# Kernel tuning notes

Hardware: AMD Instinct MI355X
Metric: run time of the kernel (lower is better)

## Reference

```python
import jax, jax.numpy as jnp
import numpy as np

RATIO = 4


def setup_inputs() -> dict:
    key = jax.random.key(0)
    ks = jax.random.split(key, 6)
    b, c, hw = 8, 64, 256
    n = (hw // RATIO) ** 2  # 4096
    return {
        "x": jax.random.normal(ks[0], (b, c, hw, hw), dtype=jnp.float32),
        "weight": jax.random.normal(ks[1], (n, n), dtype=jnp.float32) * 0.01,
        "pih_w": jax.random.normal(ks[2], (c, c, 3, 3), dtype=jnp.float32) * 0.05,
        "pih_b": jax.random.normal(ks[3], (c,), dtype=jnp.float32) * 0.05,
        "up_w": jax.random.normal(ks[4], (c, c, 4, 4), dtype=jnp.float32) * 0.05,
        "up_b": jax.random.normal(ks[5], (c,), dtype=jnp.float32) * 0.05,
    }


def reference(x, weight, pih_w, pih_b, up_w, up_b):
    b, c, h, w = x.shape
    identity = x
    # MaxPool2d(ratio)
    xp = jax.lax.reduce_window(x, -jnp.inf, jax.lax.max,
                               (1, 1, RATIO, RATIO), (1, 1, RATIO, RATIO), 'VALID')
    # 3x3 conv, pad 1
    x_pih = jax.lax.conv_general_dilated(
        xp, pih_w, window_strides=(1, 1), padding='SAME',
        dimension_numbers=('NCHW', 'OIHW', 'NCHW')) + pih_b[None, :, None, None]
    x_pih = jax.nn.relu(x_pih).reshape(b, c, -1)  # [b, c, N]
    # F.normalize(p=2, dim=2)
    nrm = jnp.sqrt(jnp.sum(x_pih * x_pih, axis=2, keepdims=True))
    nx = x_pih / jnp.maximum(nrm, 1e-12)
    # channel-channel affinity [b, c, c]
    A = jnp.einsum('bcn,bdn->bcd', nx, nx)
    # vectorized D^{-1/2}, replacing per-batch torch.diag loop
    d = 1.0 / jnp.sqrt(jnp.sum(A, axis=2) + 1e-8)  # [b, c]
    d = jnp.where(jnp.isfinite(d), d, 0.0)
    L = jnp.eye(c, dtype=x.dtype)[None] - d[:, :, None] * A * d[:, None, :]
    # diffusion: L @ x_flat @ W
    xf = xp.reshape(b, c, -1)  # [b, c, N]
    out = jnp.einsum('bcd,bdn->bcn', L, xf)
    out = jnp.einsum('bcn,nm->bcm', out, weight)
    hp, wp = h // RATIO, w // RATIO
    out = out.reshape(b, c, hp, wp)
    # ConvTranspose2d(k=4, s=4): each pixel expands to a 4x4 block
    up = jnp.einsum('bchw,coij->bohiwj', out, up_w).reshape(b, c, h, w)
    up = up + up_b[None, :, None, None]
    return jax.nn.relu(up + identity)
```

## Files before the change

kernel.cpp:

```cpp
#include <hip/hip_runtime.h>

#define NB 8
#define NC 64
#define HW 256
#define HP 64
#define NN 4096

typedef unsigned short u16;
typedef unsigned int u32;
typedef __attribute__((ext_vector_type(8))) short s16x8;
typedef __attribute__((ext_vector_type(8))) unsigned short u16x8;
typedef __attribute__((ext_vector_type(4))) float f32x4;

__device__ __forceinline__ u16 f2bf(float f) {
    unsigned u = __float_as_uint(f);
    return (u16)((u + 0x7fffu + ((u >> 16) & 1u)) >> 16);
}
__device__ __forceinline__ float bf2f(u16 v) {
    return __uint_as_float(((unsigned)v) << 16);
}

#define GLOAD16(gsrc, ldst) \
    __builtin_amdgcn_global_load_lds((const __attribute__((address_space(1))) unsigned int*)(gsrc), \
                                     (__attribute__((address_space(3))) unsigned int*)(ldst), 16, 0, 0)

__global__ __launch_bounds__(256) void prep_k(const float* __restrict__ uw,
                                              const float* __restrict__ pw,
                                              u16* __restrict__ Wb,
                                              u16* __restrict__ Bpack) {
    int bid = blockIdx.x;
    if (bid < 256) {
        int idx = bid * 256 + threadIdx.x;
        int c = idx & 63;
        int n = idx >> 6;
        int o = n >> 4, i = (n >> 2) & 3, j = n & 3;
        Wb[idx] = f2bf(uw[((c * 64 + o) * 4 + i) * 4 + j]);
    } else {
        int idx = (bid - 256) * 256 + threadIdx.x;
        if (idx >= 36864) return;
        int e = idx & 7, l = (idx >> 3) & 63, nf = (idx >> 9) & 3, s = idx >> 11;
        int ch = s & 1, kd = s >> 1;
        int dy = kd / 3, dx = kd % 3;
        int o  = nf * 16 + (l & 15);
        int ci = ch * 32 + (l >> 4) * 8 + e;
        Bpack[idx] = f2bf(pw[((o * 64 + ci) * 3 + dy) * 3 + dx]);
    }
}

__global__ __launch_bounds__(256) void transWb_k(const float* __restrict__ W,
                                                 u16* __restrict__ WTb) {
    __shared__ float tile[64 * 65];
    int k0 = blockIdx.x * 64;
    int n0 = blockIdx.y * 64;
    int t = threadIdx.x;
#pragma unroll
    for (int i = 0; i < 4; ++i) {
        int idx = t + i * 256;
        int r  = idx >> 4;
        int c4 = (idx & 15) * 4;
        float4 v = *(const float4*)&W[(long)(k0 + r) * 4096 + n0 + c4];
        tile[(c4 + 0) * 65 + r] = v.x;
        tile[(c4 + 1) * 65 + r] = v.y;
        tile[(c4 + 2) * 65 + r] = v.z;
        tile[(c4 + 3) * 65 + r] = v.w;
    }
    __syncthreads();
#pragma unroll
    for (int i = 0; i < 2; ++i) {
        int chunk = t + i * 256;
        int nr = chunk >> 3;
        int kc = (chunk & 7) * 8;
        u16x8 o;
#pragma unroll
        for (int j = 0; j < 8; ++j) o[j] = f2bf(tile[nr * 65 + kc + j]);
        *(u16x8*)&WTb[(long)(n0 + nr) * 4096 + k0 + kc] = o;
    }
}

__global__ __launch_bounds__(256) void maxpool_nhwc_k(const float* __restrict__ x,
                                                      u16* __restrict__ xpc) {
    __shared__ u16 tile[64 * 66];
    int bid = blockIdx.x;
    int b = bid >> 6, y = bid & 63;
    int t = threadIdx.x;
    int c = t >> 2, q = t & 3;
    const float* p = x + ((long)(b * 64 + c) * 256 + y * 4) * 256 + q * 64;
#pragma unroll
    for (int i = 0; i < 16; ++i) {
        float m = -3.4e38f;
#pragma unroll
        for (int r = 0; r < 4; ++r) {
            float4 v = *(const float4*)(p + r * 256 + i * 4);
            m = fmaxf(m, fmaxf(fmaxf(v.x, v.y), fmaxf(v.z, v.w)));
        }
        tile[c * 66 + q * 16 + i] = f2bf(m);
    }
    __syncthreads();
    int xo = t >> 2, cp = t & 3;
    u16x8 o0, o1;
#pragma unroll
    for (int e = 0; e < 8; ++e) o0[e] = tile[(cp * 16 + e) * 66 + xo];
#pragma unroll
    for (int e = 0; e < 8; ++e) o1[e] = tile[(cp * 16 + 8 + e) * 66 + xo];
    u16* dst = xpc + ((long)(b * 4096 + y * 64 + xo)) * 64 + cp * 16;
    *(u16x8*)dst = o0;
    *(u16x8*)(dst + 8) = o1;
}

__global__ __launch_bounds__(256) void conv_mfma_k(const u16* __restrict__ xpc,
                                                   const u16* __restrict__ Bpack,
                                                   const float* __restrict__ pb,
                                                   u16* __restrict__ xpihb) {
    __shared__ alignas(16) u16 ldsIn[3 * 66 * 64];
    int bid = blockIdx.x;
    int b = bid >> 6, y = bid & 63;
    int t = threadIdx.x;
    int w = t >> 6, l = t & 63;
    int lr = l & 15, ksub = l >> 4;

    if (t < 48) {
        int r = t >> 4, q = t & 15;
        int off = r * 8448 + (q < 8 ? q * 16 : 8320 + (q - 8) * 16);
        *(u16x8*)((char*)ldsIn + off) = (u16x8){0, 0, 0, 0, 0, 0, 0, 0};
    }
#pragma unroll
    for (int i = 0; i < 6; ++i) {
        int r  = i >> 1;
        int ya = y - 1 + r;
        int wro = (i & 1) * 4096 + t * 16;
        int dst = r * 8448 + 128 + wro;
        if (ya >= 0 && ya < 64) {
            int xsl = 1 + (wro >> 7);
            int srcoff = (wro & ~127) | ((wro & 127) ^ ((xsl & 7) << 4));
            GLOAD16((const char*)xpc + (long)(b * 64 + ya) * 8192 + srcoff,
                    (char*)ldsIn + dst);
        } else {
            *(u16x8*)((char*)ldsIn + dst) = (u16x8){0, 0, 0, 0, 0, 0, 0, 0};
        }
    }
    __syncthreads();

    f32x4 acc[4];
#pragma unroll
    for (int mf = 0; mf < 4; ++mf) acc[mf] = (f32x4){0.f, 0.f, 0.f, 0.f};

#pragma unroll
    for (int kd = 0; kd < 9; ++kd) {
        int dy = kd / 3, dx = kd % 3;
#pragma unroll
        for (int ch = 0; ch < 2; ++ch) {
            int s = kd * 2 + ch;
            s16x8 bfrag = *(const s16x8*)(Bpack + ((s * 4 + w) * 64 + l) * 8);
#pragma unroll
            for (int mf = 0; mf < 4; ++mf) {
                int xsl  = mf * 16 + lr + dx;
                int coff = (ch * 64 + ksub * 16) ^ ((xsl & 7) << 4);
                s16x8 af = *(const s16x8*)((const char*)ldsIn +
                                           dy * 8448 + xsl * 128 + coff);
                acc[mf] = __builtin_amdgcn_mfma_f32_16x16x32_bf16(
                    af, bfrag, acc[mf], 0, 0, 0);
            }
        }
    }
    int o = w * 16 + lr;
    float bias = pb[o];
    u16* dst = xpihb + ((long)(b * 64 + o)) * 4096 + y * 64;
#pragma unroll
    for (int mf = 0; mf < 4; ++mf)
#pragma unroll
        for (int rp = 0; rp < 2; ++rp) {
            u16 lo = f2bf(fmaxf(acc[mf][rp * 2]     + bias, 0.f));
            u16 hi = f2bf(fmaxf(acc[mf][rp * 2 + 1] + bias, 0.f));
            *(u32*)&dst[mf * 16 + ksub * 4 + rp * 2] = (u32)lo | ((u32)hi << 16);
        }
}

__global__ __launch_bounds__(256) void gram_mfma_k(const u16* __restrict__ xpihb,
                                                   float* __restrict__ G) {
    __shared__ alignas(16) u16 lds[64 * 128];
    int n0 = blockIdx.x * 128;
    int b  = blockIdx.y;
    int t = threadIdx.x;
    int w = t >> 6, l = t & 63;
    int lr = l & 15, ksub = l >> 4;
#pragma unroll
    for (int i = 0; i < 4; ++i) {
        int d = i * 4096 + t * 16;
        int row = d >> 8, off = d & 255;
        GLOAD16((const char*)xpihb + ((long)(b * 64 + row)) * 8192 + n0 * 2 +
                (off ^ ((row & 15) << 4)),
                (char*)lds + d);
    }
    __syncthreads();

    f32x4 acc[4];
#pragma unroll
    for (int mf = 0; mf < 4; ++mf) acc[mf] = (f32x4){0.f, 0.f, 0.f, 0.f};
#pragma unroll
    for (int kk = 0; kk < 4; ++kk) {
        int brow = w * 16 + lr;
        s16x8 bf = *(const s16x8*)((const char*)lds + brow * 256 +
                                   ((kk * 64 + ksub * 16) ^ ((brow & 15) << 4)));
#pragma unroll
        for (int mf = 0; mf < 4; ++mf) {
            int arow = mf * 16 + lr;
            s16x8 af = *(const s16x8*)((const char*)lds + arow * 256 +
                                       ((kk * 64 + ksub * 16) ^ ((arow & 15) << 4)));
            acc[mf] = __builtin_amdgcn_mfma_f32_16x16x32_bf16(af, bf, acc[mf], 0, 0, 0);
        }
    }
    float* Gb = G + b * 4096;
#pragma unroll
    for (int mf = 0; mf < 4; ++mf)
#pragma unroll
        for (int r = 0; r < 4; ++r)
            atomicAdd(&Gb[(mf * 16 + (l >> 4) * 4 + r) * 64 + w * 16 + lr],
                      acc[mf][r]);
}

__global__ void build_L_k(const float* __restrict__ G, u16* __restrict__ Lb16) {
    int b = blockIdx.x;
    int c = threadIdx.x;
    __shared__ float nrm[64], dvv[64];
    const float* Gb = G + b * 4096;
    float n = sqrtf(Gb[c * 64 + c]);
    n = fmaxf(n, 1e-12f);
    nrm[c] = n;
    __syncthreads();
    float rs = 0.f;
    for (int d = 0; d < 64; ++d) rs += Gb[c * 64 + d] / (n * nrm[d]);
    float dd = 1.0f / sqrtf(rs + 1e-8f);
    if (!(dd <= 3.0e38f)) dd = 0.0f;
    dvv[c] = dd;
    __syncthreads();
    for (int d = 0; d < 64; ++d) {
        float A = Gb[c * 64 + d] / (n * nrm[d]);
        float val = ((c == d) ? 1.0f : 0.0f) - dd * A * dvv[d];
        Lb16[(b * 64 + c) * 64 + d] = f2bf(val);
    }
}

__global__ __launch_bounds__(256) void diffuse_mfma_k(const u16* __restrict__ Lb16,
                                                      const u16* __restrict__ xpc,
                                                      u16* __restrict__ Ab16) {
    __shared__ alignas(16) u16 lds[128 * 64];
    int n0 = blockIdx.x * 128;
    int b  = blockIdx.y;
    int t = threadIdx.x;
    int w = t >> 6, l = t & 63;
    int lr = l & 15, ksub = l >> 4;
#pragma unroll
    for (int i = 0; i < 4; ++i) {
        int d = i * 4096 + t * 16;
        int row = d >> 7, off = d & 127;
        GLOAD16((const char*)xpc + ((long)(b * 4096 + n0 + row)) * 128 +
                (off ^ ((row & 7) << 4)),
                (char*)lds + d);
    }
    __syncthreads();

    const u16* Lb = Lb16 + b * 4096;
    f32x4 acc[4][2];
#pragma unroll
    for (int mf = 0; mf < 4; ++mf)
#pragma unroll
        for (int nq = 0; nq < 2; ++nq) acc[mf][nq] = (f32x4){0.f, 0.f, 0.f, 0.f};

#pragma unroll
    for (int kk = 0; kk < 2; ++kk) {
        s16x8 bfr[2];
#pragma unroll
        for (int nq = 0; nq < 2; ++nq) {
            int brow = w * 32 + nq * 16 + lr;
            bfr[nq] = *(const s16x8*)((const char*)lds + brow * 128 +
                                      ((kk * 64 + ksub * 16) ^ ((brow & 7) << 4)));
        }
#pragma unroll
        for (int mf = 0; mf < 4; ++mf) {
            s16x8 af = *(const s16x8*)(Lb + (mf * 16 + lr) * 64 + kk * 32 + ksub * 8);
#pragma unroll
            for (int nq = 0; nq < 2; ++nq)
                acc[mf][nq] = __builtin_amdgcn_mfma_f32_16x16x32_bf16(
                    af, bfr[nq], acc[mf][nq], 0, 0, 0);
        }
    }
#pragma unroll
    for (int mf = 0; mf < 4; ++mf)
#pragma unroll
        for (int nq = 0; nq < 2; ++nq)
#pragma unroll
            for (int r = 0; r < 4; ++r)
                Ab16[((long)(b * 64 + mf * 16 + (l >> 4) * 4 + r)) * 4096 +
                     n0 + w * 32 + nq * 16 + lr] = f2bf(acc[mf][nq][r]);
}

#define KSPLIT 4
#define KSLICE 1024
__global__ __launch_bounds__(256) void gemm_mfma_k(const u16* __restrict__ A,
                                                   const u16* __restrict__ WT,
                                                   u16* __restrict__ Cp) {
    __shared__ alignas(16) u16 ldsA[2][8192];
    __shared__ alignas(16) u16 ldsB[2][8192];
    int bid = blockIdx.x;
    int swz = (bid & 7) * 64 + (bid >> 3);
    int m0 = (swz & 3) * 128;
    int n0 = ((swz >> 2) & 31) * 128;
    int z  = swz >> 7;
    int t = threadIdx.x;
    int w = t >> 6, l = t & 63;
    int wr = w >> 1, wc = w & 1;
    int lr = l & 15;
    int lk = (l >> 4) << 4;

    f32x4 acc[4][4];
#pragma unroll
    for (int mf = 0; mf < 4; ++mf)
#pragma unroll
        for (int nf = 0; nf < 4; ++nf) acc[mf][nf] = (f32x4){0.f, 0.f, 0.f, 0.f};

    const char* Ab = (const char*)(A  + (long)m0 * 4096 + z * KSLICE);
    const char* Bb = (const char*)(WT + (long)n0 * 4096 + z * KSLICE);

    auto stage = [&](int buf, int k0) {
#pragma unroll
        for (int i = 0; i < 4; ++i) {
            int d   = i * 4096 + t * 16;
            int row = d >> 7;
            int off = d & 127;
            int sk  = off ^ ((row & 7) << 4);
            GLOAD16(Ab + (long)row * 8192 + k0 * 2 + sk, (char*)ldsA[buf] + d);
            GLOAD16(Bb + (long)row * 8192 + k0 * 2 + sk, (char*)ldsB[buf] + d);
        }
    };

    stage(0, 0);
    __syncthreads();
    int cur = 0;
    for (int k0 = 0; k0 < KSLICE; k0 += 64) {
        if (k0 + 64 < KSLICE) stage(cur ^ 1, k0 + 64);
#pragma unroll
        for (int kk = 0; kk < 2; ++kk) {
            s16x8 af[4], bf[4];
#pragma unroll
            for (int f = 0; f < 4; ++f) {
                int ar = wr * 64 + f * 16 + lr;
                af[f] = *(const s16x8*)((const char*)ldsA[cur] + ar * 128 +
                                        ((kk * 64 + lk) ^ ((ar & 7) << 4)));
                int br = wc * 64 + f * 16 + lr;
                bf[f] = *(const s16x8*)((const char*)ldsB[cur] + br * 128 +
                                        ((kk * 64 + lk) ^ ((br & 7) << 4)));
            }
#pragma unroll
            for (int mf = 0; mf < 4; ++mf)
#pragma unroll
                for (int nf = 0; nf < 4; ++nf)
                    acc[mf][nf] = __builtin_amdgcn_mfma_f32_16x16x32_bf16(
                        af[mf], bf[nf], acc[mf][nf], 0, 0, 0);
        }
        __syncthreads();
        cur ^= 1;
    }
    u16* Cz = Cp + (long)z * 2097152;
#pragma unroll
    for (int mf = 0; mf < 4; ++mf)
#pragma unroll
        for (int nf = 0; nf < 4; ++nf)
#pragma unroll
            for (int r = 0; r < 4; ++r) {
                int row = m0 + wr * 64 + mf * 16 + (l >> 4) * 4 + r;
                int col = n0 + wc * 64 + nf * 16 + lr;
                Cz[(long)row * 4096 + col] = f2bf(acc[mf][nf][r]);
            }
}

__global__ __launch_bounds__(256) void reduce4T_k(const u16* __restrict__ Cp,
                                                  u16* __restrict__ A2) {
    __shared__ float xs[64 * 65];
    int n0 = blockIdx.x * 64;
    int b  = blockIdx.y;
    int t = threadIdx.x;
    int c = t >> 2, seg = t & 3;
    float s[16];
#pragma unroll
    for (int k = 0; k < 16; ++k) s[k] = 0.f;
#pragma unroll
    for (int z = 0; z < KSPLIT; ++z) {
        const u16* p = Cp + ((long)z * 512 + b * 64 + c) * 4096 + n0 + seg * 16;
        u16x8 v0 = *(const u16x8*)p;
        u16x8 v1 = *(const u16x8*)(p + 8);
#pragma unroll
        for (int k = 0; k < 8; ++k) {
            s[k]     += bf2f(v0[k]);
            s[8 + k] += bf2f(v1[k]);
        }
    }
#pragma unroll
    for (int k = 0; k < 16; ++k) xs[c * 65 + seg * 16 + k] = s[k];
    __syncthreads();
    int n = t >> 2, q = t & 3;
    u16x8 o0, o1;
#pragma unroll
    for (int k = 0; k < 8; ++k) o0[k] = f2bf(xs[(q * 16 + k) * 65 + n]);
#pragma unroll
    for (int k = 0; k < 8; ++k) o1[k] = f2bf(xs[(q * 16 + 8 + k) * 65 + n]);
    u16* dst = A2 + ((long)b * 4096 + n0 + n) * 64 + q * 16;
    *(u16x8*)dst = o0;
    *(u16x8*)(dst + 8) = o1;
}

__global__ __launch_bounds__(256) void convT_mfma_k(const u16* __restrict__ A2,
                                                    const u16* __restrict__ Wb,
                                                    const float* __restrict__ ub,
                                                    const float* __restrict__ x,
                                                    float* __restrict__ out) {
    __shared__ alignas(16) char smem[34816];
    u16*   ldsA = (u16*)smem;
    u16*   ldsB = (u16*)(smem + 16384);
    float* ldsC = (float*)smem;
    int mt = blockIdx.x;
    int nt = blockIdx.y;
    int m0 = mt * 128;
    int n0 = nt * 128;
    int t = threadIdx.x;
    int w = t >> 6, l = t & 63;
    int wr = w >> 1, wc = w & 1;
    int lr = l & 15;
    int lkb = (l >> 4) << 4;

    const char* Ab = (const char*)(A2 + (long)m0 * 64);
    const char* Bb = (const char*)(Wb + (long)n0 * 64);
#pragma unroll
    for (int i = 0; i < 4; ++i) {
        int d = i * 4096 + t * 16;
        int srcoff = (d & ~127) | ((d & 127) ^ (((d >> 7) & 7) << 4));
        GLOAD16(Ab + srcoff, (char*)ldsA + d);
        GLOAD16(Bb + srcoff, (char*)ldsB + d);
    }
    __syncthreads();

    f32x4 acc[4][4];
#pragma unroll
    for (int mf = 0; mf < 4; ++mf)
#pragma unroll
        for (int nf = 0; nf < 4; ++nf) acc[mf][nf] = (f32x4){0.f, 0.f, 0.f, 0.f};

#pragma unroll
    for (int kk = 0; kk < 2; ++kk) {
        s16x8 af[4], bfg[4];
#pragma unroll
        for (int f = 0; f < 4; ++f) {
            int ar = wr * 64 + f * 16 + lr;
            af[f] = *(const s16x8*)((const char*)ldsA + ar * 128 +
                                    ((kk * 64 + lkb) ^ ((ar & 7) << 4)));
            int br = wc * 64 + f * 16 + lr;
            bfg[f] = *(const s16x8*)((const char*)ldsB + br * 128 +
                                     ((kk * 64 + lkb) ^ ((br & 7) << 4)));
        }
#pragma unroll
        for (int mf = 0; mf < 4; ++mf)
#pragma unroll
            for (int nf = 0; nf < 4; ++nf)
                acc[mf][nf] = __builtin_amdgcn_mfma_f32_16x16x32_bf16(
                    af[mf], bfg[nf], acc[mf][nf], 0, 0, 0);
    }
    __syncthreads();

#pragma unroll
    for (int nh = 0; nh < 2; ++nh) {
        if (nh) __syncthreads();
        if (wc == nh) {
#pragma unroll
            for (int mf = 0; mf < 4; ++mf)
#pragma unroll
                for (int nf = 0; nf < 4; ++nf)
#pragma unroll
                    for (int r = 0; r < 4; ++r) {
                        int row = wr * 64 + mf * 16 + (l >> 4) * 4 + r;
                        int col = nf * 16 + lr;
                        ldsC[row * 68 + (col ^ (((row >> 3) & 7) << 2))] =
                            acc[mf][nf][r];
                    }
        }
        __syncthreads();
#pragma unroll
        for (int q = 0; q < 2; ++q) {
            int idx = q * 256 + t;
            int ml = idx & 127;
            int oo = idx >> 7;
            int o  = nt * 8 + nh * 4 + oo;
            float bias = ub[o];
            int mg = m0 + ml;
            int b = mg >> 12, pix = mg & 4095;
            int h = pix >> 6, ww = pix & 63;
            long base = ((long)(b * 64 + o) * 256 + h * 4) * 256 + ww * 4;
#pragma unroll
            for (int i = 0; i < 4; ++i) {
                f32x4 cv = *(const f32x4*)&ldsC[ml * 68 +
                            ((oo * 16 + i * 4) ^ (((ml >> 3) & 7) << 2))];
                float4 xi = *(const float4*)&x[base + i * 256];
                float4 rr;
                rr.x = fmaxf(cv[0] + bias + xi.x, 0.f);
                rr.y = fmaxf(cv[1] + bias + xi.y, 0.f);
                rr.z = fmaxf(cv[2] + bias + xi.z, 0.f);
                rr.w = fmaxf(cv[3] + bias + xi.w, 0.f);
                *(float4*)&out[base + i * 256] = rr;
            }
        }
    }
}

extern "C" void kernel_launch(void* const* d_in, const int* in_sizes, int n_in,
                              void* d_out, int out_size, void* d_ws, size_t ws_size,
                              hipStream_t stream) {
    const float* x      = (const float*)d_in[0];
    const float* weight = (const float*)d_in[1];
    const float* pih_w  = (const float*)d_in[2];
    const float* pih_b  = (const float*)d_in[3];
    const float* up_w   = (const float*)d_in[4];
    const float* up_b   = (const float*)d_in[5];
    float* out = (float*)d_out;
    float* ws  = (float*)d_ws;

    u16*   xpc   = (u16*)ws;
    u16*   xpihb = (u16*)(ws + 2097152);
    u16*   Ab16  = (u16*)(ws + 3145728);
    float* G     = ws + 4194304;
    u16*   Lb16  = (u16*)(ws + 4227072);
    u16*   Wb    = (u16*)(ws + 4259840);
    u16*   WTb   = (u16*)(ws + 4325376);
    u16*   Cp    = (u16*)(ws + 12713984);
    u16*   Bpack = Cp + 2097152;
    u16*   A2    = (u16*)ws;

    hipMemsetAsync(G, 0, 32768 * sizeof(float), stream);
    prep_k        <<<400, 256, 0, stream>>>(up_w, pih_w, Wb, Bpack);
    transWb_k     <<<dim3(64, 64), 256, 0, stream>>>(weight, WTb);
    maxpool_nhwc_k<<<512, 256, 0, stream>>>(x, xpc);
    conv_mfma_k   <<<512, 256, 0, stream>>>(xpc, Bpack, pih_b, xpihb);
    gram_mfma_k   <<<dim3(32, 8), 256, 0, stream>>>(xpihb, G);
    build_L_k     <<<8, 64, 0, stream>>>(G, Lb16);
    diffuse_mfma_k<<<dim3(32, 8), 256, 0, stream>>>(Lb16, xpc, Ab16);
    gemm_mfma_k   <<<512, 256, 0, stream>>>(Ab16, WTb, Cp);
    reduce4T_k    <<<dim3(64, 8), 256, 0, stream>>>(Cp, A2);
    convT_mfma_k  <<<dim3(256, 8), 256, 0, stream>>>(A2, Wb, up_b, x, out);
}
```

Measured before the change: 190.5 us.

## Merge front kernels, fold L build into diffuse, tile-major split-K partials

```diff
diff --git a/kernel.cpp b/kernel.cpp
--- a/kernel.cpp
+++ b/kernel.cpp
@@ -24,87 +24,88 @@
     __builtin_amdgcn_global_load_lds((const __attribute__((address_space(1))) unsigned int*)(gsrc), \
                                      (__attribute__((address_space(3))) unsigned int*)(ldst), 16, 0, 0)
 
-__global__ __launch_bounds__(256) void prep_k(const float* __restrict__ uw,
-                                              const float* __restrict__ pw,
-                                              u16* __restrict__ Wb,
-                                              u16* __restrict__ Bpack) {
+__global__ __launch_bounds__(256) void front_k(const float* __restrict__ x,
+                                               const float* __restrict__ W,
+                                               const float* __restrict__ uw,
+                                               const float* __restrict__ pw,
+                                               u16* __restrict__ xpc,
+                                               u16* __restrict__ WTb,
+                                               u16* __restrict__ Wb,
+                                               u16* __restrict__ Bpack) {
+    __shared__ alignas(16) char sm[16640];
     int bid = blockIdx.x;
-    if (bid < 256) {
-        int idx = bid * 256 + threadIdx.x;
-        int c = idx & 63;
-        int n = idx >> 6;
-        int o = n >> 4, i = (n >> 2) & 3, j = n & 3;
-        Wb[idx] = f2bf(uw[((c * 64 + o) * 4 + i) * 4 + j]);
+    int t = threadIdx.x;
+    if (bid < 512) {
+        u16* tile = (u16*)sm;
+        int b = bid >> 6, y = bid & 63;
+        int c = t >> 2, q = t & 3;
+        const float* p = x + ((long)(b * 64 + c) * 256 + y * 4) * 256 + q * 64;
+#pragma unroll
+        for (int i = 0; i < 16; ++i) {
+            float m = -3.4e38f;
+#pragma unroll
+            for (int r = 0; r < 4; ++r) {
+                float4 v = *(const float4*)(p + r * 256 + i * 4);
+                m = fmaxf(m, fmaxf(fmaxf(v.x, v.y), fmaxf(v.z, v.w)));
+            }
+            tile[c * 66 + q * 16 + i] = f2bf(m);
+        }
+        __syncthreads();
+        int xo = t >> 2, cp = t & 3;
+        u16x8 o0, o1;
+#pragma unroll
+        for (int e = 0; e < 8; ++e) o0[e] = tile[(cp * 16 + e) * 66 + xo];
+#pragma unroll
+        for (int e = 0; e < 8; ++e) o1[e] = tile[(cp * 16 + 8 + e) * 66 + xo];
+        u16* dst = xpc + ((long)(b * 4096 + y * 64 + xo)) * 64 + cp * 16;
+        *(u16x8*)dst = o0;
+        *(u16x8*)(dst + 8) = o1;
+    } else if (bid < 4608) {
+        float* tile = (float*)sm;
+        int tb = bid - 512;
+        int k0 = (tb & 63) * 64;
+        int n0 = (tb >> 6) * 64;
+#pragma unroll
+        for (int i = 0; i < 4; ++i) {
+            int idx = t + i * 256;
+            int r  = idx >> 4;
+            int c4 = (idx & 15) * 4;
+            float4 v = *(const float4*)&W[(long)(k0 + r) * 4096 + n0 + c4];
+            tile[(c4 + 0) * 65 + r] = v.x;
+            tile[(c4 + 1) * 65 + r] = v.y;
+            tile[(c4 + 2) * 65 + r] = v.z;
+            tile[(c4 + 3) * 65 + r] = v.w;
+        }
+        __syncthreads();
+#pragma unroll
+        for (int i = 0; i < 2; ++i) {
+            int chunk = t + i * 256;
+            int nr = chunk >> 3;
+            int kc = (chunk & 7) * 8;
+            u16x8 o;
+#pragma unroll
+            for (int j = 0; j < 8; ++j) o[j] = f2bf(tile[nr * 65 + kc + j]);
+            *(u16x8*)&WTb[(long)(n0 + nr) * 4096 + k0 + kc] = o;
+        }
     } else {
-        int idx = (bid - 256) * 256 + threadIdx.x;
-        if (idx >= 36864) return;
-        int e = idx & 7, l = (idx >> 3) & 63, nf = (idx >> 9) & 3, s = idx >> 11;
-        int ch = s & 1, kd = s >> 1;
-        int dy = kd / 3, dx = kd % 3;
-        int o  = nf * 16 + (l & 15);
-        int ci = ch * 32 + (l >> 4) * 8 + e;
-        Bpack[idx] = f2bf(pw[((o * 64 + ci) * 3 + dy) * 3 + dx]);
-    }
-}
-
-__global__ __launch_bounds__(256) void transWb_k(const float* __restrict__ W,
-                                                 u16* __restrict__ WTb) {
-    __shared__ float tile[64 * 65];
-    int k0 = blockIdx.x * 64;
-    int n0 = blockIdx.y * 64;
-    int t = threadIdx.x;
-#pragma unroll
-    for (int i = 0; i < 4; ++i) {
-        int idx = t + i * 256;
-        int r  = idx >> 4;
-        int c4 = (idx & 15) * 4;
-        float4 v = *(const float4*)&W[(long)(k0 + r) * 4096 + n0 + c4];
-        tile[(c4 + 0) * 65 + r] = v.x;
-        tile[(c4 + 1) * 65 + r] = v.y;
-        tile[(c4 + 2) * 65 + r] = v.z;
-        tile[(c4 + 3) * 65 + r] = v.w;
-    }
-    __syncthreads();
-#pragma unroll
-    for (int i = 0; i < 2; ++i) {
-        int chunk = t + i * 256;
-        int nr = chunk >> 3;
-        int kc = (chunk & 7) * 8;
-        u16x8 o;
-#pragma unroll
-        for (int j = 0; j < 8; ++j) o[j] = f2bf(tile[nr * 65 + kc + j]);
-        *(u16x8*)&WTb[(long)(n0 + nr) * 4096 + k0 + kc] = o;
-    }
-}
-
-__global__ __launch_bounds__(256) void maxpool_nhwc_k(const float* __restrict__ x,
-                                                      u16* __restrict__ xpc) {
-    __shared__ u16 tile[64 * 66];
-    int bid = blockIdx.x;
-    int b = bid >> 6, y = bid & 63;
-    int t = threadIdx.x;
-    int c = t >> 2, q = t & 3;
-    const float* p = x + ((long)(b * 64 + c) * 256 + y * 4) * 256 + q * 64;
-#pragma unroll
-    for (int i = 0; i < 16; ++i) {
-        float m = -3.4e38f;
-#pragma unroll
-        for (int r = 0; r < 4; ++r) {
-            float4 v = *(const float4*)(p + r * 256 + i * 4);
-            m = fmaxf(m, fmaxf(fmaxf(v.x, v.y), fmaxf(v.z, v.w)));
-        }
-        tile[c * 66 + q * 16 + i] = f2bf(m);
-    }
-    __syncthreads();
-    int xo = t >> 2, cp = t & 3;
-    u16x8 o0, o1;
-#pragma unroll
-    for (int e = 0; e < 8; ++e) o0[e] = tile[(cp * 16 + e) * 66 + xo];
-#pragma unroll
-    for (int e = 0; e < 8; ++e) o1[e] = tile[(cp * 16 + 8 + e) * 66 + xo];
-    u16* dst = xpc + ((long)(b * 4096 + y * 64 + xo)) * 64 + cp * 16;
-    *(u16x8*)dst = o0;
-    *(u16x8*)(dst + 8) = o1;
+        int pbid = bid - 4608;
+        if (pbid < 256) {
+            int idx = pbid * 256 + t;
+            int c = idx & 63;
+            int n = idx >> 6;
+            int o = n >> 4, i = (n >> 2) & 3, j = n & 3;
+            Wb[idx] = f2bf(uw[((c * 64 + o) * 4 + i) * 4 + j]);
+        } else {
+            int idx = (pbid - 256) * 256 + t;
+            if (idx >= 36864) return;
+            int e = idx & 7, l = (idx >> 3) & 63, nf = (idx >> 9) & 3, s = idx >> 11;
+            int ch = s & 1, kd = s >> 1;
+            int dy = kd / 3, dx = kd % 3;
+            int o  = nf * 16 + (l & 15);
+            int ci = ch * 32 + (l >> 4) * 8 + e;
+            Bpack[idx] = f2bf(pw[((o * 64 + ci) * 3 + dy) * 3 + dx]);
+        }
+    }
 }
 
 __global__ __launch_bounds__(256) void conv_mfma_k(const u16* __restrict__ xpc,
@@ -218,37 +219,18 @@
                       acc[mf][r]);
 }
 
-__global__ void build_L_k(const float* __restrict__ G, u16* __restrict__ Lb16) {
-    int b = blockIdx.x;
-    int c = threadIdx.x;
-    __shared__ float nrm[64], dvv[64];
-    const float* Gb = G + b * 4096;
-    float n = sqrtf(Gb[c * 64 + c]);
-    n = fmaxf(n, 1e-12f);
-    nrm[c] = n;
-    __syncthreads();
-    float rs = 0.f;
-    for (int d = 0; d < 64; ++d) rs += Gb[c * 64 + d] / (n * nrm[d]);
-    float dd = 1.0f / sqrtf(rs + 1e-8f);
-    if (!(dd <= 3.0e38f)) dd = 0.0f;
-    dvv[c] = dd;
-    __syncthreads();
-    for (int d = 0; d < 64; ++d) {
-        float A = Gb[c * 64 + d] / (n * nrm[d]);
-        float val = ((c == d) ? 1.0f : 0.0f) - dd * A * dvv[d];
-        Lb16[(b * 64 + c) * 64 + d] = f2bf(val);
-    }
-}
-
-__global__ __launch_bounds__(256) void diffuse_mfma_k(const u16* __restrict__ Lb16,
+__global__ __launch_bounds__(256) void diffuse_mfma_k(const float* __restrict__ G,
                                                       const u16* __restrict__ xpc,
                                                       u16* __restrict__ Ab16) {
     __shared__ alignas(16) u16 lds[128 * 64];
+    __shared__ alignas(16) u16 ldsL[64 * 64];
+    __shared__ float nrm[64], dvv[64];
     int n0 = blockIdx.x * 128;
     int b  = blockIdx.y;
     int t = threadIdx.x;
     int w = t >> 6, l = t & 63;
     int lr = l & 15, ksub = l >> 4;
+
 #pragma unroll
     for (int i = 0; i < 4; ++i) {
         int d = i * 4096 + t * 16;
@@ -257,9 +239,36 @@
                 (off ^ ((row & 7) << 4)),
                 (char*)lds + d);
     }
-    __syncthreads();
-
-    const u16* Lb = Lb16 + b * 4096;
+
+    const float* Gb = G + b * 4096;
+    if (t < 64) nrm[t] = fmaxf(sqrtf(Gb[t * 64 + t]), 1e-12f);
+    __syncthreads();
+    if (t < 64) {
+        float nc = nrm[t];
+        float rs = 0.f;
+        for (int d = 0; d < 64; ++d) rs += Gb[t * 64 + d] / (nc * nrm[d]);
+        float dd = 1.0f / sqrtf(rs + 1e-8f);
+        if (!(dd <= 3.0e38f)) dd = 0.0f;
+        dvv[t] = dd;
+    }
+    __syncthreads();
+    {
+        int c = t >> 2;
+        int dbase = (t & 3) * 16;
+        float nc = nrm[c], dc = dvv[c];
+#pragma unroll
+        for (int dp2 = 0; dp2 < 8; ++dp2) {
+            int d0 = dbase + dp2 * 2;
+            float A0 = Gb[c * 64 + d0]     / (nc * nrm[d0]);
+            float A1 = Gb[c * 64 + d0 + 1] / (nc * nrm[d0 + 1]);
+            float v0 = ((c == d0)     ? 1.f : 0.f) - dc * A0 * dvv[d0];
+            float v1 = ((c == d0 + 1) ? 1.f : 0.f) - dc * A1 * dvv[d0 + 1];
+            int o = c * 64 + (d0 ^ ((c & 7) << 3));
+            *(u32*)&ldsL[o] = (u32)f2bf(v0) | ((u32)f2bf(v1) << 16);
+        }
+    }
+    __syncthreads();
+
     f32x4 acc[4][2];
 #pragma unroll
     for (int mf = 0; mf < 4; ++mf)
@@ -277,7 +286,9 @@
         }
 #pragma unroll
         for (int mf = 0; mf < 4; ++mf) {
-            s16x8 af = *(const s16x8*)(Lb + (mf * 16 + lr) * 64 + kk * 32 + ksub * 8);
+            int arow = mf * 16 + lr;
+            s16x8 af = *(const s16x8*)((const char*)ldsL + arow * 128 +
+                                       ((kk * 64 + ksub * 16) ^ ((arow & 7) << 4)));
 #pragma unroll
             for (int nq = 0; nq < 2; ++nq)
                 acc[mf][nq] = __builtin_amdgcn_mfma_f32_16x16x32_bf16(
@@ -360,52 +371,74 @@
         __syncthreads();
         cur ^= 1;
     }
-    u16* Cz = Cp + (long)z * 2097152;
+    int tile = (swz & 3) * 32 + ((swz >> 2) & 31);
+    u16 carr[64];
 #pragma unroll
     for (int mf = 0; mf < 4; ++mf)
 #pragma unroll
         for (int nf = 0; nf < 4; ++nf)
 #pragma unroll
-            for (int r = 0; r < 4; ++r) {
-                int row = m0 + wr * 64 + mf * 16 + (l >> 4) * 4 + r;
-                int col = n0 + wc * 64 + nf * 16 + lr;
-                Cz[(long)row * 4096 + col] = f2bf(acc[mf][nf][r]);
-            }
+            for (int r = 0; r < 4; ++r)
+                carr[mf * 16 + nf * 4 + r] = f2bf(acc[mf][nf][r]);
+    u16* dp = Cp + ((long)(z * 128 + tile) * 256 + t) * 64;
+#pragma unroll
+    for (int v8 = 0; v8 < 8; ++v8)
+        *(u16x8*)&dp[v8 * 8] = *(const u16x8*)&carr[v8 * 8];
 }
 
 __global__ __launch_bounds__(256) void reduce4T_k(const u16* __restrict__ Cp,
                                                   u16* __restrict__ A2) {
-    __shared__ float xs[64 * 65];
-    int n0 = blockIdx.x * 64;
-    int b  = blockIdx.y;
-    int t = threadIdx.x;
-    int c = t >> 2, seg = t & 3;
-    float s[16];
-#pragma unroll
-    for (int k = 0; k < 16; ++k) s[k] = 0.f;
+    __shared__ u16 ldsT[128 * 128];
+    int tile = blockIdx.x;
+    int tm = tile >> 5, tn = tile & 31;
+    int n0 = tn * 128;
+    int t = threadIdx.x;
+    int w = t >> 6, l = t & 63;
+    int wr = w >> 1, wc = w & 1, lr = l & 15;
+
+    float s[64];
+#pragma unroll
+    for (int mf = 0; mf < 4; ++mf)
+#pragma unroll
+        for (int nf = 0; nf < 4; ++nf)
+#pragma unroll
+            for (int r = 0; r < 4; ++r) s[mf * 16 + nf * 4 + r] = 0.f;
+
+    const u16* dp = Cp + ((long)tile * 256 + t) * 64;
 #pragma unroll
     for (int z = 0; z < KSPLIT; ++z) {
-        const u16* p = Cp + ((long)z * 512 + b * 64 + c) * 4096 + n0 + seg * 16;
-        u16x8 v0 = *(const u16x8*)p;
-        u16x8 v1 = *(const u16x8*)(p + 8);
-#pragma unroll
-        for (int k = 0; k < 8; ++k) {
-            s[k]     += bf2f(v0[k]);
-            s[8 + k] += bf2f(v1[k]);
-        }
-    }
-#pragma unroll
-    for (int k = 0; k < 16; ++k) xs[c * 65 + seg * 16 + k] = s[k];
-    __syncthreads();
-    int n = t >> 2, q = t & 3;
-    u16x8 o0, o1;
-#pragma unroll
-    for (int k = 0; k < 8; ++k) o0[k] = f2bf(xs[(q * 16 + k) * 65 + n]);
-#pragma unroll
-    for (int k = 0; k < 8; ++k) o1[k] = f2bf(xs[(q * 16 + 8 + k) * 65 + n]);
-    u16* dst = A2 + ((long)b * 4096 + n0 + n) * 64 + q * 16;
-    *(u16x8*)dst = o0;
-    *(u16x8*)(dst + 8) = o1;
+        const u16* pz = dp + (long)z * 128 * 256 * 64;
+#pragma unroll
+        for (int v8 = 0; v8 < 8; ++v8) {
+            u16x8 vv = *(const u16x8*)&pz[v8 * 8];
+#pragma unroll
+            for (int e = 0; e < 8; ++e) s[v8 * 8 + e] += bf2f(vv[e]);
+        }
+    }
+#pragma unroll
+    for (int mf = 0; mf < 4; ++mf)
+#pragma unroll
+        for (int nf = 0; nf < 4; ++nf) {
+            int mbase = wr * 64 + mf * 16 + (l >> 4) * 4;
+            int pix   = wc * 64 + nf * 16 + lr;
+            int g = (mbase >> 3) ^ (pix & 7);
+            int o = pix * 128 + g * 8 + (mbase & 7);
+            u32 w0 = (u32)f2bf(s[mf * 16 + nf * 4 + 0]) |
+                     ((u32)f2bf(s[mf * 16 + nf * 4 + 1]) << 16);
+            u32 w1 = (u32)f2bf(s[mf * 16 + nf * 4 + 2]) |
+                     ((u32)f2bf(s[mf * 16 + nf * 4 + 3]) << 16);
+            *(u32*)&ldsT[o]     = w0;
+            *(u32*)&ldsT[o + 2] = w1;
+        }
+    __syncthreads();
+    int pix_l = t >> 1, bh = t & 1;
+    u16* dst = A2 + ((long)((2 * tm + bh) * 4096 + n0 + pix_l)) * 64;
+#pragma unroll
+    for (int gg = 0; gg < 8; ++gg) {
+        int q = bh * 8 + gg;
+        u16x8 vv = *(const u16x8*)&ldsT[pix_l * 128 + (q ^ (pix_l & 7)) * 8];
+        *(u16x8*)&dst[gg * 8] = vv;
+    }
 }
 
 __global__ __launch_bounds__(256) void convT_mfma_k(const u16* __restrict__ A2,
@@ -525,7 +558,6 @@
     u16*   xpihb = (u16*)(ws + 2097152);
     u16*   Ab16  = (u16*)(ws + 3145728);
     float* G     = ws + 4194304;
-    u16*   Lb16  = (u16*)(ws + 4227072);
     u16*   Wb    = (u16*)(ws + 4259840);
     u16*   WTb   = (u16*)(ws + 4325376);
     u16*   Cp    = (u16*)(ws + 12713984);
@@ -533,14 +565,12 @@
     u16*   A2    = (u16*)ws;
 
     hipMemsetAsync(G, 0, 32768 * sizeof(float), stream);
-    prep_k        <<<400, 256, 0, stream>>>(up_w, pih_w, Wb, Bpack);
-    transWb_k     <<<dim3(64, 64), 256, 0, stream>>>(weight, WTb);
-    maxpool_nhwc_k<<<512, 256, 0, stream>>>(x, xpc);
+    front_k       <<<5008, 256, 0, stream>>>(x, weight, up_w, pih_w,
+                                             xpc, WTb, Wb, Bpack);
     conv_mfma_k   <<<512, 256, 0, stream>>>(xpc, Bpack, pih_b, xpihb);
     gram_mfma_k   <<<dim3(32, 8), 256, 0, stream>>>(xpihb, G);
-    build_L_k     <<<8, 64, 0, stream>>>(G, Lb16);
-    diffuse_mfma_k<<<dim3(32, 8), 256, 0, stream>>>(Lb16, xpc, Ab16);
+    diffuse_mfma_k<<<dim3(32, 8), 256, 0, stream>>>(G, xpc, Ab16);
     gemm_mfma_k   <<<512, 256, 0, stream>>>(Ab16, WTb, Cp);
-    reduce4T_k    <<<dim3(64, 8), 256, 0, stream>>>(Cp, A2);
+    reduce4T_k    <<<128, 256, 0, stream>>>(Cp, A2);
     convT_mfma_k  <<<dim3(256, 8), 256, 0, stream>>>(A2, Wb, up_b, x, out);
 }
```

After: 202.2 us. +6.1%, slower.
